# Kernel optimization log

Measured on AMD Instinct MI355X. Metric: run time of the kernel, lower is better.

The kernel has to match this reference:

```python
import jax, jax.numpy as jnp
import numpy as np

B, T, F, H, C = 128, 16, 1024, 1024, 2513


def setup_inputs() -> dict:
    key = jax.random.key(0)
    ks = jax.random.split(key, 11)
    s = 1.0 / np.sqrt(H)

    def u(k, shape):
        return jax.random.uniform(k, shape, jnp.float32, -s, s)

    return {
        "inputs": jax.random.normal(ks[0], (B, T, F), jnp.float32),
        "Wi_r": u(ks[1], (4 * H, F)),
        "Wh_r": u(ks[2], (4 * H, H)),
        "bi_r": u(ks[3], (4 * H,)),
        "bh_r": u(ks[4], (4 * H,)),
        "Wi_u": u(ks[5], (4 * H, F)),
        "Wh_u": u(ks[6], (4 * H, H)),
        "bi_u": u(ks[7], (4 * H,)),
        "bh_u": u(ks[8], (4 * H,)),
        "Wc": u(ks[9], (C, H)),
        "bc": u(ks[10], (C,)),
    }


def _lstm_gates(pre, c):
    # pre: [..., 4H] pre-activations; torch gate order i, f, g, o
    i, f, g, o = jnp.split(pre, 4, axis=-1)
    c_new = jax.nn.sigmoid(f) * c + jax.nn.sigmoid(i) * jnp.tanh(g)
    h_new = jax.nn.sigmoid(o) * jnp.tanh(c_new)
    return h_new, c_new


def reference(inputs, Wi_r, Wh_r, bi_r, bh_r, Wi_u, Wh_u, bi_u, bh_u, Wc, bc):
    # Dropout layers are identity (eval mode).
    x = inputs.transpose(1, 0, 2)  # [T, B, F]
    Tn, Bn = x.shape[0], x.shape[1]
    Hd = Wh_r.shape[1]

    # ---- rolling LSTM: collect hidden & cell at every timestep ----
    def roll_step(carry, xt):
        h, c = carry
        pre = xt @ Wi_r.T + h @ Wh_r.T + (bi_r + bh_r)
        h, c = _lstm_gates(pre, c)
        return (h, c), (h, c)

    h0 = jnp.zeros((Bn, Hd), x.dtype)
    _, (hs, cs) = jax.lax.scan(roll_step, (h0, h0), x)  # each [T, B, H]

    # ---- unrolling LSTM: for each t, feed x[t] repeated (T - t + 1) times,
    # starting from (hs[t], cs[t]); take hidden at the last step.
    # Vectorized over t: the input is constant per step, so precompute its projection.
    xi = x @ Wi_u.T + (bi_u + bh_u)  # [T, B, 4H]

    def unroll_step(carry, _):
        h, c = carry  # [T, B, H]
        pre = xi + h @ Wh_u.T
        h, c = _lstm_gates(pre, c)
        return (h, c), h

    _, hs_un = jax.lax.scan(unroll_step, (hs, cs), None, length=Tn + 1)  # [T+1, T, B, H]
    # sequence for start t has length L = T - t + 1, so last hidden is step index T - t
    idx = Tn - jnp.arange(Tn)
    h_n = hs_un[idx, jnp.arange(Tn)]  # [T, B, H]

    xcls = h_n.transpose(1, 0, 2)  # [B, T, H]
    y = xcls @ Wc.T + bc  # [B, T, num_class]
    return y
```

## Files before the change

kernel.cpp:

```cpp
#include <hip/hip_runtime.h>
#include <cstdint>

using half_t = _Float16;
using half8  = __attribute__((ext_vector_type(8))) _Float16;
using half4v = __attribute__((ext_vector_type(4))) _Float16;
using f32x4  = __attribute__((ext_vector_type(4))) float;
using flt4v  = __attribute__((ext_vector_type(4))) float;

namespace {
constexpr int kT = 16, kH = 1024, kFH = 4096, kC = 2513, kCP = 2560;
constexpr int kSlot = 128 * 1024;
constexpr int kPar  = 17 * kSlot;
}

__device__ __forceinline__ void gload16(const void* g, void* l) {
  __builtin_amdgcn_global_load_lds((const __attribute__((address_space(1))) void*)g,
                                   (__attribute__((address_space(3))) void*)l, 16, 0, 0);
}
__device__ __forceinline__ float sgm(float x) { return 1.0f / (1.0f + __expf(-x)); }

__global__ void setup_all(const flt4v* __restrict__ WiR, const flt4v* __restrict__ WhR,
                          const flt4v* __restrict__ WiU, const flt4v* __restrict__ WhU,
                          const flt4v* __restrict__ Wc, const float* __restrict__ x,
                          const float* __restrict__ biR, const float* __restrict__ bhR,
                          const float* __restrict__ biU, const float* __restrict__ bhU,
                          const float* __restrict__ bc,
                          half4v* __restrict__ WiRh, half4v* __restrict__ WhRh,
                          half4v* __restrict__ WiUh, half4v* __restrict__ WhUh,
                          half4v* __restrict__ Wch, half_t* __restrict__ xh,
                          float* __restrict__ br_p, float* __restrict__ bu_p,
                          float* __restrict__ bcp) {
  int blk = blockIdx.x;
  if (blk < 18944) {
    long i = (long)blk * 256 + threadIdx.x;
    const long Q = 1048576;
    if (i < Q) { WiRh[i] = __builtin_convertvector(WiR[i], half4v); return; }
    i -= Q;
    if (i < Q) { WhRh[i] = __builtin_convertvector(WhR[i], half4v); return; }
    i -= Q;
    if (i < Q) { WiUh[i] = __builtin_convertvector(WiU[i], half4v); return; }
    i -= Q;
    if (i < Q) { WhUh[i] = __builtin_convertvector(WhU[i], half4v); return; }
    i -= Q;
    if (i < (long)kC * kH / 4) {
      Wch[i] = __builtin_convertvector(Wc[i], half4v);
    } else if (i < (long)kCP * kH / 4) {
      half4v z = {(_Float16)0, (_Float16)0, (_Float16)0, (_Float16)0};
      Wch[i] = z;
    }
    return;
  }
  blk -= 18944;
  if (blk < 2048) {
    int t = blk >> 7, b = blk & 127;
    const flt4v* src = (const flt4v*)(x + ((long)b * kT + t) * kH);
    half4v* dst = (half4v*)(xh + (long)blk * kH);
    dst[threadIdx.x] = __builtin_convertvector(src[threadIdx.x], half4v);
    return;
  }
  blk -= 2048;
  {
    int i = blk * 256 + threadIdx.x;
    if (i < kFH) {
      int j = i >> 2, gt = i & 3;
      br_p[i] = biR[gt * kH + j] + bhR[gt * kH + j];
      bu_p[i] = biU[gt * kH + j] + bhU[gt * kH + j];
    }
    if (i < kCP) bcp[i] = (i < kC) ? bc[i] : 0.0f;
  }
}

__device__ __forceinline__ int brow_gate(int r, int j0) {
  return (((r >> 4) & 3) << 10) + j0 + ((r >> 6) << 4) + (r & 15);
}

template <int MR>
__device__ __forceinline__ void gemm_core(
    const half_t* __restrict__ A, const half_t* __restrict__ B,
    const long* ao, const long* bo, half_t* AsB, half_t* BsB,
    int tid, int wm, int wc, int row16, int g, f32x4 acc[][4]) {
  constexpr int UA = MR / 32;
  constexpr int ABUF = MR * 64;
#pragma unroll
  for (int i = 0; i < UA; ++i) gload16(A + ao[i], AsB + (i * 256 + tid) * 8);
#pragma unroll
  for (int i = 0; i < 4; ++i) gload16(B + bo[i], BsB + (i * 256 + tid) * 8);
  __syncthreads();
  int p = 0;
  for (int kt = 64; kt <= 1024; kt += 64) {
    if (kt < 1024) {
      half_t* as_n = AsB + (p ^ 1) * ABUF;
      half_t* bs_n = BsB + (p ^ 1) * 8192;
#pragma unroll
      for (int i = 0; i < UA; ++i) gload16(A + ao[i] + kt, as_n + (i * 256 + tid) * 8);
#pragma unroll
      for (int i = 0; i < 4; ++i) gload16(B + bo[i] + kt, bs_n + (i * 256 + tid) * 8);
    }
    const half_t* as_ = AsB + p * ABUF;
    const half_t* bs_ = BsB + p * 8192;
#pragma unroll
    for (int s = 0; s < 2; ++s) {
      half8 af[UA], bf[4];
#pragma unroll
      for (int a = 0; a < UA; ++a) {
        const int row = wm * (MR / 2) + (a << 4) + row16;
        const int slot = (s * 4 + g) ^ (row & 7);
        af[a] = *(const half8*)&as_[row * 64 + slot * 8];
      }
#pragma unroll
      for (int b = 0; b < 4; ++b) {
        const int row = (wc << 6) + (b << 4) + row16;
        const int slot = (s * 4 + g) ^ (row & 7);
        bf[b] = *(const half8*)&bs_[row * 64 + slot * 8];
      }
#pragma unroll
      for (int a = 0; a < UA; ++a)
#pragma unroll
        for (int b = 0; b < 4; ++b)
          acc[a][b] = __builtin_amdgcn_mfma_f32_16x16x32_f16(af[a], bf[b], acc[a][b], 0, 0, 0);
    }
    __syncthreads();
    p ^= 1;
  }
}

template <int MR>
__global__ __launch_bounds__(256, (MR == 64 ? 3 : 2)) void pipe_step(
    const int u, const int nRec, const int projBase,
    const half_t* __restrict__ xh,
    const half_t* __restrict__ WiRh, const half_t* __restrict__ WiUh,
    const float* __restrict__ brp, const float* __restrict__ bup,
    const half_t* __restrict__ Wr, const half_t* __restrict__ Wu,
    half_t* __restrict__ xiR, half_t* __restrict__ xiU,
    half_t* __restrict__ Hbuf, float* __restrict__ Cbuf) {
  __shared__ __align__(16) half_t As[2 * MR * 64];
  __shared__ __align__(16) half_t Bs[2 * 8192];
  constexpr int FA = MR / 32;
  const int tid = threadIdx.x;
  const int lane = tid & 63;
  const int w = tid >> 6, wm = w >> 1, wc = w & 1;
  const int row16 = lane & 15;
  const int g = lane >> 4;
  const int j0 = blockIdx.x << 5;
  const int sy = blockIdx.y;
  const int seg = (MR == 64) ? (sy >> 1) : sy;
  const int mrow0 = (MR == 64) ? ((sy & 1) << 6) : 0;

  f32x4 acc[FA][4];
  const f32x4 z4 = {0.f, 0.f, 0.f, 0.f};
#pragma unroll
  for (int a = 0; a < FA; ++a)
#pragma unroll
    for (int b = 0; b < 4; ++b) acc[a][b] = z4;

  int srow[4], skk[4];
#pragma unroll
  for (int i = 0; i < 4; ++i) {
    srow[i] = i * 32 + (tid >> 3);
    skk[i] = ((tid & 7) ^ (srow[i] & 7)) * 8;
  }

  if (seg < nRec) {
    const bool isRoll = (u <= 16) && (seg == 0);
    const int c = (u <= 16) ? (seg - 1) : seg;
    const int pr = (u & 1) ^ 1, pw = u & 1;
    const int slot_in_raw = isRoll ? (u - 2) : c;
    const bool zeroA = (slot_in_raw < 0);
    const int slot_in = zeroA ? 0 : slot_in_raw;
    const int slot_out = isRoll ? (u - 1) : c;
    const half_t* A  = Hbuf + (size_t)pr * kPar + (size_t)slot_in * kSlot;
    const float* Cin = Cbuf + (size_t)pr * kPar + (size_t)slot_in * kSlot;
    half_t* Ho = Hbuf + (size_t)pw * kPar + (size_t)slot_out * kSlot;
    float*  Co = Cbuf + (size_t)pw * kPar + (size_t)slot_out * kSlot;
    const half_t* W  = isRoll ? Wr : Wu;
    const half_t* xi = isRoll ? (xiR + (size_t)(u - 1) * 524288)
                              : (xiU + (size_t)c * 524288);

    if (!zeroA) {
      long ao[FA], bo[4];
#pragma unroll
      for (int i = 0; i < FA; ++i) ao[i] = (long)(mrow0 + srow[i]) * kH + skk[i];
#pragma unroll
      for (int i = 0; i < 4; ++i) bo[i] = (long)brow_gate(srow[i], j0) * kH + skk[i];
      gemm_core<MR>(A, W, ao, bo, As, Bs, tid, wm, wc, row16, g, acc);
    }

    const int jg = j0 + (wc << 4) + row16;
#pragma unroll
    for (int a = 0; a < FA; ++a) {
      const int mb = mrow0 + wm * (MR / 2) + (a << 4) + (g << 2);
#pragma unroll
      for (int r = 0; r < 4; ++r) {
        const int m = mb + r;
        const half4v xv = *(const half4v*)&xi[((long)m * kH + jg) * 4];
        const float pi = acc[a][0][r] + (float)xv[0];
        const float pf = acc[a][1][r] + (float)xv[1];
        const float pg = acc[a][2][r] + (float)xv[2];
        const float po = acc[a][3][r] + (float)xv[3];
        const float co = zeroA ? 0.0f : Cin[(long)m * kH + jg];
        const float cn = sgm(pf) * co + sgm(pi) * tanhf(pg);
        const float hn = sgm(po) * tanhf(cn);
        Ho[(long)m * kH + jg] = (half_t)hn;
        Co[(long)m * kH + jg] = cn;
      }
    }
  } else {
    const int p = projBase + (seg - nRec);
    int z, rr;
    if (p == 0)       { z = 0; rr = 0; }
    else if (p == 1)  { z = 1; rr = 0; }
    else if (p <= 16) { z = 0; rr = p - 1; }
    else              { z = 1; rr = p - 16; }
    const half_t* Wt = z ? WiUh : WiRh;
    const float* bias_p = z ? bup : brp;
    half_t* xi = z ? xiU : xiR;
    const int m0 = (rr << 7) + mrow0;

    long ao[FA], bo[4];
#pragma unroll
    for (int i = 0; i < FA; ++i) ao[i] = (long)(m0 + srow[i]) * kH + skk[i];
#pragma unroll
    for (int i = 0; i < 4; ++i) bo[i] = (long)brow_gate(srow[i], j0) * kH + skk[i];
    gemm_core<MR>(xh, Wt, ao, bo, As, Bs, tid, wm, wc, row16, g, acc);

    const int jg = j0 + (wc << 4) + row16;
    const f32x4 bv = *(const f32x4*)&bias_p[jg * 4];
#pragma unroll
    for (int a = 0; a < FA; ++a) {
      const int mb = m0 + wm * (MR / 2) + (a << 4) + (g << 2);
#pragma unroll
      for (int r4 = 0; r4 < 4; ++r4) {
        half4v o;
        o[0] = (half_t)(acc[a][0][r4] + bv[0]);
        o[1] = (half_t)(acc[a][1][r4] + bv[1]);
        o[2] = (half_t)(acc[a][2][r4] + bv[2]);
        o[3] = (half_t)(acc[a][3][r4] + bv[3]);
        *(half4v*)&xi[((long)(mb + r4) * kH + jg) * 4] = o;
      }
    }
  }
}

__global__ __launch_bounds__(256, 3) void cls_gemm(
    const half_t* __restrict__ Hfin, const half_t* __restrict__ Wcw,
    const float* __restrict__ bcp, float* __restrict__ out) {
  __shared__ __align__(16) half_t As[2 * 4096];
  __shared__ __align__(16) half_t Bs[2 * 8192];
  const int tid = threadIdx.x;
  const int lane = tid & 63;
  const int w = tid >> 6, wm = w >> 1, wc = w & 1;
  const int row16 = lane & 15;
  const int g = lane >> 4;
  const int n00 = blockIdx.x << 7;
  const int t = blockIdx.y >> 1;
  const int m0 = (t << 7) + ((blockIdx.y & 1) << 6);

  int srow[4], skk[4];
#pragma unroll
  for (int i = 0; i < 4; ++i) {
    srow[i] = i * 32 + (tid >> 3);
    skk[i] = ((tid & 7) ^ (srow[i] & 7)) * 8;
  }
  long ao[2], bo[4];
#pragma unroll
  for (int i = 0; i < 2; ++i) ao[i] = (long)(m0 + srow[i]) * kH + skk[i];
#pragma unroll
  for (int i = 0; i < 4; ++i) bo[i] = (long)(n00 + srow[i]) * kH + skk[i];

  f32x4 acc[2][4];
  const f32x4 z4 = {0.f, 0.f, 0.f, 0.f};
#pragma unroll
  for (int a = 0; a < 2; ++a)
#pragma unroll
    for (int b = 0; b < 4; ++b) acc[a][b] = z4;

  gemm_core<64>(Hfin, Wcw, ao, bo, As, Bs, tid, wm, wc, row16, g, acc);

#pragma unroll
  for (int a = 0; a < 2; ++a) {
    const int mb = m0 + wm * 32 + (a << 4) + (g << 2);
#pragma unroll
    for (int b = 0; b < 4; ++b) {
      const int n = n00 + (wc << 6) + (b << 4) + row16;
      if (n < kC) {
        const float bvv = bcp[n];
#pragma unroll
        for (int r = 0; r < 4; ++r) {
          const int m = mb + r;
          const int bi = m & 127;
          out[((long)bi * kT + t) * kC + n] = acc[a][b][r] + bvv;
        }
      }
    }
  }
}

extern "C" void kernel_launch(void* const* d_in, const int* in_sizes, int n_in,
                              void* d_out, int out_size, void* d_ws, size_t ws_size,
                              hipStream_t stream) {
  const float* x   = (const float*)d_in[0];
  const float* WiR = (const float*)d_in[1];
  const float* WhR = (const float*)d_in[2];
  const float* biR = (const float*)d_in[3];
  const float* bhR = (const float*)d_in[4];
  const float* WiU = (const float*)d_in[5];
  const float* WhU = (const float*)d_in[6];
  const float* biU = (const float*)d_in[7];
  const float* bhU = (const float*)d_in[8];
  const float* Wc  = (const float*)d_in[9];
  const float* bc  = (const float*)d_in[10];

  size_t off = 0;
  auto alloc = [&](size_t bytes) -> void* {
    void* p = (char*)d_ws + off;
    off += (bytes + 255) & ~(size_t)255;
    return p;
  };
  half_t* xh   = (half_t*)alloc((size_t)2048 * 1024 * 2);
  half_t* WiRh = (half_t*)alloc((size_t)4096 * 1024 * 2);
  half_t* WhRh = (half_t*)alloc((size_t)4096 * 1024 * 2);
  half_t* WiUh = (half_t*)alloc((size_t)4096 * 1024 * 2);
  half_t* WhUh = (half_t*)alloc((size_t)4096 * 1024 * 2);
  half_t* Wch  = (half_t*)alloc((size_t)2560 * 1024 * 2);
  float*  br   = (float*)alloc(4096 * 4);
  float*  bu   = (float*)alloc(4096 * 4);
  float*  bcp  = (float*)alloc(2560 * 4);
  half_t* xiR  = (half_t*)alloc((size_t)2048 * 4096 * 2);
  half_t* xiU  = (half_t*)alloc((size_t)2048 * 4096 * 2);
  half_t* Hbuf = (half_t*)alloc((size_t)2 * kPar * 2);
  float*  Cbuf = (float*)alloc((size_t)2 * kPar * 4);
  float*  outp = (float*)d_out;
  (void)ws_size; (void)in_sizes; (void)n_in; (void)out_size;

  setup_all<<<21008, 256, 0, stream>>>(
      (const flt4v*)WiR, (const flt4v*)WhR, (const flt4v*)WiU, (const flt4v*)WhU,
      (const flt4v*)Wc, x, biR, bhR, biU, bhU, bc,
      (half4v*)WiRh, (half4v*)WhRh, (half4v*)WiUh, (half4v*)WhUh, (half4v*)Wch,
      xh, br, bu, bcp);

  pipe_step<64><<<dim3(32, 6), 256, 0, stream>>>(
      0, 0, 0, xh, WiRh, WiUh, br, bu, WhRh, WhUh, xiR, xiU, Hbuf, Cbuf);

  for (int u = 1; u <= 18; ++u) {
    const int nchain = (u >= 2) ? ((u - 2 < 15 ? u - 2 : 15) + 1) : 0;
    const int nRec = (u <= 16 ? 1 : 0) + nchain;
    int projBase = 0, nProj = 0;
    if (u == 1) { projBase = 3;  nProj = 11; }
    if (u == 2) { projBase = 14; nProj = 10; }
    if (u == 3) { projBase = 24; nProj = 8;  }
    if (u <= 12) {
      pipe_step<64><<<dim3(32, 2 * (nRec + nProj)), 256, 0, stream>>>(
          u, nRec, projBase, xh, WiRh, WiUh, br, bu, WhRh, WhUh, xiR, xiU,
          Hbuf, Cbuf);
    } else {
      pipe_step<128><<<dim3(32, nRec), 256, 0, stream>>>(
          u, nRec, 0, xh, WiRh, WiUh, br, bu, WhRh, WhUh, xiR, xiU,
          Hbuf, Cbuf);
    }
  }

  cls_gemm<<<dim3(20, 32), 256, 0, stream>>>(Hbuf, Wch, bcp, (float*)outp);
}
```

Baseline: 501.9 us.

## Halve GEMM K-tile to 32, always use 64-row tiles, raise occupancy to four

The shared GEMM core now stages 32-wide K slices instead of 64, with a new XOR swizzle and per-thread load mapping (one A load, two B loads per stage). This halves LDS use per block, so launch bounds rise to 4 blocks per CU for both the step and classifier kernels. The 128-row variant used for late recurrent steps is removed, so every step launches 64-row half-tiles and late steps get twice as many blocks. The cost is twice as many K iterations and barriers, with less MFMA work per sync.

```diff
diff --git a/kernel.cpp b/kernel.cpp
--- a/kernel.cpp
+++ b/kernel.cpp
@@ -79,53 +79,49 @@
     const half_t* __restrict__ A, const half_t* __restrict__ B,
     const long* ao, const long* bo, half_t* AsB, half_t* BsB,
     int tid, int wm, int wc, int row16, int g, f32x4 acc[][4]) {
-  constexpr int UA = MR / 32;
-  constexpr int ABUF = MR * 64;
+  constexpr int UA = MR / 64;
+  constexpr int ABUF = MR * 32;
 #pragma unroll
   for (int i = 0; i < UA; ++i) gload16(A + ao[i], AsB + (i * 256 + tid) * 8);
 #pragma unroll
-  for (int i = 0; i < 4; ++i) gload16(B + bo[i], BsB + (i * 256 + tid) * 8);
+  for (int i = 0; i < 2; ++i) gload16(B + bo[i], BsB + (i * 256 + tid) * 8);
   __syncthreads();
   int p = 0;
-  for (int kt = 64; kt <= 1024; kt += 64) {
+  for (int kt = 32; kt <= 1024; kt += 32) {
     if (kt < 1024) {
       half_t* as_n = AsB + (p ^ 1) * ABUF;
-      half_t* bs_n = BsB + (p ^ 1) * 8192;
+      half_t* bs_n = BsB + (p ^ 1) * 4096;
 #pragma unroll
       for (int i = 0; i < UA; ++i) gload16(A + ao[i] + kt, as_n + (i * 256 + tid) * 8);
 #pragma unroll
-      for (int i = 0; i < 4; ++i) gload16(B + bo[i] + kt, bs_n + (i * 256 + tid) * 8);
+      for (int i = 0; i < 2; ++i) gload16(B + bo[i] + kt, bs_n + (i * 256 + tid) * 8);
     }
     const half_t* as_ = AsB + p * ABUF;
-    const half_t* bs_ = BsB + p * 8192;
-#pragma unroll
-    for (int s = 0; s < 2; ++s) {
-      half8 af[UA], bf[4];
-#pragma unroll
-      for (int a = 0; a < UA; ++a) {
-        const int row = wm * (MR / 2) + (a << 4) + row16;
-        const int slot = (s * 4 + g) ^ (row & 7);
-        af[a] = *(const half8*)&as_[row * 64 + slot * 8];
-      }
-#pragma unroll
-      for (int b = 0; b < 4; ++b) {
-        const int row = (wc << 6) + (b << 4) + row16;
-        const int slot = (s * 4 + g) ^ (row & 7);
-        bf[b] = *(const half8*)&bs_[row * 64 + slot * 8];
-      }
-#pragma unroll
-      for (int a = 0; a < UA; ++a)
-#pragma unroll
-        for (int b = 0; b < 4; ++b)
-          acc[a][b] = __builtin_amdgcn_mfma_f32_16x16x32_f16(af[a], bf[b], acc[a][b], 0, 0, 0);
-    }
+    const half_t* bs_ = BsB + p * 4096;
+    half8 af[MR / 32], bf[4];
+#pragma unroll
+    for (int a = 0; a < MR / 32; ++a) {
+      const int row = wm * (MR / 2) + (a << 4) + row16;
+      const int slot = g ^ ((row >> 1) & 3);
+      af[a] = *(const half8*)&as_[row * 32 + slot * 8];
+    }
+#pragma unroll
+    for (int b = 0; b < 4; ++b) {
+      const int row = (wc << 6) + (b << 4) + row16;
+      const int slot = g ^ ((row >> 1) & 3);
+      bf[b] = *(const half8*)&bs_[row * 32 + slot * 8];
+    }
+#pragma unroll
+    for (int a = 0; a < MR / 32; ++a)
+#pragma unroll
+      for (int b = 0; b < 4; ++b)
+        acc[a][b] = __builtin_amdgcn_mfma_f32_16x16x32_f16(af[a], bf[b], acc[a][b], 0, 0, 0);
     __syncthreads();
     p ^= 1;
   }
 }
 
-template <int MR>
-__global__ __launch_bounds__(256, (MR == 64 ? 3 : 2)) void pipe_step(
+__global__ __launch_bounds__(256, 4) void pipe_step(
     const int u, const int nRec, const int projBase,
     const half_t* __restrict__ xh,
     const half_t* __restrict__ WiRh, const half_t* __restrict__ WiUh,
@@ -133,9 +129,9 @@
     const half_t* __restrict__ Wr, const half_t* __restrict__ Wu,
     half_t* __restrict__ xiR, half_t* __restrict__ xiU,
     half_t* __restrict__ Hbuf, float* __restrict__ Cbuf) {
-  __shared__ __align__(16) half_t As[2 * MR * 64];
-  __shared__ __align__(16) half_t Bs[2 * 8192];
-  constexpr int FA = MR / 32;
+  constexpr int MR = 64, FA = 2;
+  __shared__ __align__(16) half_t As[2 * MR * 32];
+  __shared__ __align__(16) half_t Bs[2 * 128 * 32];
   const int tid = threadIdx.x;
   const int lane = tid & 63;
   const int w = tid >> 6, wm = w >> 1, wc = w & 1;
@@ -143,8 +139,8 @@
   const int g = lane >> 4;
   const int j0 = blockIdx.x << 5;
   const int sy = blockIdx.y;
-  const int seg = (MR == 64) ? (sy >> 1) : sy;
-  const int mrow0 = (MR == 64) ? ((sy & 1) << 6) : 0;
+  const int seg = sy >> 1;
+  const int mrow0 = (sy & 1) << 6;
 
   f32x4 acc[FA][4];
   const f32x4 z4 = {0.f, 0.f, 0.f, 0.f};
@@ -153,12 +149,8 @@
 #pragma unroll
     for (int b = 0; b < 4; ++b) acc[a][b] = z4;
 
-  int srow[4], skk[4];
-#pragma unroll
-  for (int i = 0; i < 4; ++i) {
-    srow[i] = i * 32 + (tid >> 3);
-    skk[i] = ((tid & 7) ^ (srow[i] & 7)) * 8;
-  }
+  const int sr = tid >> 2;
+  const int kk = ((tid & 3) ^ ((sr >> 1) & 3)) * 8;
 
   if (seg < nRec) {
     const bool isRoll = (u <= 16) && (seg == 0);
@@ -177,11 +169,10 @@
                               : (xiU + (size_t)c * 524288);
 
     if (!zeroA) {
-      long ao[FA], bo[4];
-#pragma unroll
-      for (int i = 0; i < FA; ++i) ao[i] = (long)(mrow0 + srow[i]) * kH + skk[i];
-#pragma unroll
-      for (int i = 0; i < 4; ++i) bo[i] = (long)brow_gate(srow[i], j0) * kH + skk[i];
+      long ao[1], bo[2];
+      ao[0] = (long)(mrow0 + sr) * kH + kk;
+      bo[0] = (long)brow_gate(sr, j0) * kH + kk;
+      bo[1] = (long)brow_gate(sr + 64, j0) * kH + kk;
       gemm_core<MR>(A, W, ao, bo, As, Bs, tid, wm, wc, row16, g, acc);
     }
 
@@ -216,11 +207,10 @@
     half_t* xi = z ? xiU : xiR;
     const int m0 = (rr << 7) + mrow0;
 
-    long ao[FA], bo[4];
-#pragma unroll
-    for (int i = 0; i < FA; ++i) ao[i] = (long)(m0 + srow[i]) * kH + skk[i];
-#pragma unroll
-    for (int i = 0; i < 4; ++i) bo[i] = (long)brow_gate(srow[i], j0) * kH + skk[i];
+    long ao[1], bo[2];
+    ao[0] = (long)(m0 + sr) * kH + kk;
+    bo[0] = (long)brow_gate(sr, j0) * kH + kk;
+    bo[1] = (long)brow_gate(sr + 64, j0) * kH + kk;
     gemm_core<MR>(xh, Wt, ao, bo, As, Bs, tid, wm, wc, row16, g, acc);
 
     const int jg = j0 + (wc << 4) + row16;
@@ -241,11 +231,11 @@
   }
 }
 
-__global__ __launch_bounds__(256, 3) void cls_gemm(
+__global__ __launch_bounds__(256, 4) void cls_gemm(
     const half_t* __restrict__ Hfin, const half_t* __restrict__ Wcw,
     const float* __restrict__ bcp, float* __restrict__ out) {
-  __shared__ __align__(16) half_t As[2 * 4096];
-  __shared__ __align__(16) half_t Bs[2 * 8192];
+  __shared__ __align__(16) half_t As[2 * 64 * 32];
+  __shared__ __align__(16) half_t Bs[2 * 128 * 32];
   const int tid = threadIdx.x;
   const int lane = tid & 63;
   const int w = tid >> 6, wm = w >> 1, wc = w & 1;
@@ -255,17 +245,12 @@
   const int t = blockIdx.y >> 1;
   const int m0 = (t << 7) + ((blockIdx.y & 1) << 6);
 
-  int srow[4], skk[4];
-#pragma unroll
-  for (int i = 0; i < 4; ++i) {
-    srow[i] = i * 32 + (tid >> 3);
-    skk[i] = ((tid & 7) ^ (srow[i] & 7)) * 8;
-  }
-  long ao[2], bo[4];
-#pragma unroll
-  for (int i = 0; i < 2; ++i) ao[i] = (long)(m0 + srow[i]) * kH + skk[i];
-#pragma unroll
-  for (int i = 0; i < 4; ++i) bo[i] = (long)(n00 + srow[i]) * kH + skk[i];
+  const int sr = tid >> 2;
+  const int kk = ((tid & 3) ^ ((sr >> 1) & 3)) * 8;
+  long ao[1], bo[2];
+  ao[0] = (long)(m0 + sr) * kH + kk;
+  bo[0] = (long)(n00 + sr) * kH + kk;
+  bo[1] = (long)(n00 + sr + 64) * kH + kk;
 
   f32x4 acc[2][4];
   const f32x4 z4 = {0.f, 0.f, 0.f, 0.f};
@@ -338,7 +323,7 @@
       (half4v*)WiRh, (half4v*)WhRh, (half4v*)WiUh, (half4v*)WhUh, (half4v*)Wch,
       xh, br, bu, bcp);
 
-  pipe_step<64><<<dim3(32, 6), 256, 0, stream>>>(
+  pipe_step<<<dim3(32, 6), 256, 0, stream>>>(
       0, 0, 0, xh, WiRh, WiUh, br, bu, WhRh, WhUh, xiR, xiU, Hbuf, Cbuf);
 
   for (int u = 1; u <= 18; ++u) {
@@ -348,15 +333,9 @@
     if (u == 1) { projBase = 3;  nProj = 11; }
     if (u == 2) { projBase = 14; nProj = 10; }
     if (u == 3) { projBase = 24; nProj = 8;  }
-    if (u <= 12) {
-      pipe_step<64><<<dim3(32, 2 * (nRec + nProj)), 256, 0, stream>>>(
-          u, nRec, projBase, xh, WiRh, WiUh, br, bu, WhRh, WhUh, xiR, xiU,
-          Hbuf, Cbuf);
-    } else {
-      pipe_step<128><<<dim3(32, nRec), 256, 0, stream>>>(
-          u, nRec, 0, xh, WiRh, WiUh, br, bu, WhRh, WhUh, xiR, xiU,
-          Hbuf, Cbuf);
-    }
+    pipe_step<<<dim3(32, 2 * (nRec + nProj)), 256, 0, stream>>>(
+        u, nRec, projBase, xh, WiRh, WiUh, br, bu, WhRh, WhUh, xiR, xiU,
+        Hbuf, Cbuf);
   }
 
   cls_gemm<<<dim3(20, 32), 256, 0, stream>>>(Hbuf, Wch, bcp, (float*)outp);
```

Result: slower. 570.7 us (+13.7%).
